# Kernel optimization log

Measured on AMD Instinct MI355X. Metric: run time of the kernel, lower is better.

The kernel has to match this reference:

```python
import jax, jax.numpy as jnp
import numpy as np

INF = 1.0e6  # 'infinity' for squared EDT; max real value is ~3*128^2 ~ 5e4


def edt_1d_sq(f, axis):
    """One pass of Felzenszwalb separable squared EDT along `axis`.
    d[i] = min_j f[j] + (i - j)^2  (brute-force vectorized lower envelope)."""
    f = jnp.moveaxis(f, axis, -1)
    n = f.shape[-1]
    i = jnp.arange(n, dtype=f.dtype)
    sq = (i[:, None] - i[None, :]) ** 2  # (n, n)
    d = jnp.min(f[..., None, :] + sq, axis=-1)  # (..., n)
    return jnp.moveaxis(d, -1, axis)


def compute_fg_dtm(mask):
    """Euclidean distance transform of foreground (distance to nearest background),
    matching scipy.ndimage.distance_transform_edt applied per batch element on the
    (C, X, Y, Z) mask (C==1 so the channel axis pass is the identity).
    mask: bool (B, 1, X, Y, Z) -> float32 (B, 1, X, Y, Z)."""
    def per_b(m):
        g = jnp.where(m, jnp.float32(INF), jnp.float32(0.0))
        for ax in range(m.ndim):
            g = edt_1d_sq(g, ax)
        return jnp.sqrt(g)
    return jax.lax.map(per_b, mask)


def setup_inputs() -> dict:
    key = jax.random.key(0)
    k1, k2, k3 = jax.random.split(key, 3)
    B, C, X, Y, Z = 2, 2, 128, 128, 128
    return {
        "outputs": jax.random.normal(k1, (B, C, X, Y, Z), dtype=jnp.float32),
        "outputs_dist": jax.random.normal(k2, (B, C, X, Y, Z), dtype=jnp.float32) * 10.0,
        "y": jax.random.randint(k3, (B, 1, X, Y, Z), 0, 2),
        "distance_map_weight": 1.0,
    }


def reference(outputs, outputs_dist, y, distance_map_weight):
    n_pred_ch = outputs.shape[1]
    # MONAI one_hot: (B,1,X,Y,Z) int labels -> (B,C,X,Y,Z) float
    y1h = jnp.moveaxis(jax.nn.one_hot(y[:, 0], n_pred_ch, dtype=outputs.dtype), -1, 1)
    x = outputs[:, 1:]            # foreground logits (B, 1, X, Y, Z)
    t = y1h[:, 1:]                # foreground mask
    od = outputs_dist[:, 1:]
    gt_dis = compute_fg_dtm(t > 0.5)
    # BCE with logits (mean reduction), numerically stable
    loss_ce = jnp.mean(jnp.maximum(x, 0.0) - x * t + jnp.log1p(jnp.exp(-jnp.abs(x))))
    # dice loss, flattened per batch element
    N = x.shape[0]
    smooth = jnp.float32(1.0)
    p = jax.nn.sigmoid(x).reshape(N, -1)
    tf = t.reshape(N, -1)
    dice = (2.0 * jnp.sum(p * tf, axis=1) + smooth) / (jnp.sum(p, axis=1) + jnp.sum(tf, axis=1) + smooth)
    loss_dice = 1.0 - jnp.sum(dice) / N
    # weighted L1 on the distance head, masked by the foreground mask
    msum = jnp.sum(t)
    loss_dist = jnp.where(
        msum == 0,
        jnp.float32(0.0),
        jnp.sum(jnp.abs(od - gt_dis) * t) / jnp.maximum(msum, jnp.float32(1e-12)),
    )
    return loss_ce + loss_dice + distance_map_weight * loss_dist
```

## Files before the change

### kernel.cpp

```cpp
#include <hip/hip_runtime.h>
#include <math.h>

#define M_SPATIAL 2097152
#define MV4 (M_SPATIAL / 4)

__device__ __forceinline__ float wave_redf(float v) {
#pragma unroll
  for (int o = 32; o > 0; o >>= 1) v += __shfl_down(v, o, 64);
  return v;
}
__device__ __forceinline__ double wave_redd(double v) {
#pragma unroll
  for (int o = 32; o > 0; o >>= 1) v += __shfl_down(v, o, 64);
  return v;
}


__global__ __launch_bounds__(256) void kA_ce(const float4* __restrict__ outputs4,
                                             const int4* __restrict__ y4,
                                             double* __restrict__ part) {
  int blk = blockIdx.x;
  int base = blk * 1024;
  int b = (blk >= 512) ? 1 : 0;
  const float4* xc = outputs4 + (size_t)(b * 2 + 1) * MV4;
  float ce = 0.f, ps = 0.f, pts = 0.f, tsum = 0.f;
#pragma unroll
  for (int k = 0; k < 4; ++k) {
    int v4 = base + (int)threadIdx.x + k * 256;
    int s4 = v4 & (MV4 - 1);
    int4 yv = y4[v4];
    float4 x = xc[s4];
#define ELEM(c, yc)                                                         \
    {                                                                       \
      float t = (yc == 1) ? 1.0f : 0.0f;                                    \
      float xx = x.c;                                                       \
      ce += fmaxf(xx, 0.0f) - xx * t + log1pf(expf(-fabsf(xx)));            \
      float p = 1.0f / (1.0f + expf(-xx));                                  \
      ps += p; pts += p * t; tsum += t;                                     \
    }
    ELEM(x, yv.x) ELEM(y, yv.y) ELEM(z, yv.z) ELEM(w, yv.w)
#undef ELEM
  }
  float r0 = wave_redf(ce), r1 = wave_redf(ps), r2 = wave_redf(pts), r3 = wave_redf(tsum);
  __shared__ float sm[4][4];
  int lane = threadIdx.x & 63, w = threadIdx.x >> 6;
  if (lane == 0) { sm[w][0] = r0; sm[w][1] = r1; sm[w][2] = r2; sm[w][3] = r3; }
  __syncthreads();
  if (threadIdx.x == 0) {
    part[blk]        = (double)(sm[0][0] + sm[1][0] + sm[2][0] + sm[3][0]);
    part[1024 + blk] = (double)(sm[0][1] + sm[1][1] + sm[2][1] + sm[3][1]);
    part[2048 + blk] = (double)(sm[0][2] + sm[1][2] + sm[2][2] + sm[3][2]);
    part[3072 + blk] = (double)(sm[0][3] + sm[1][3] + sm[2][3] + sm[3][3]);
  }
}

__global__ __launch_bounds__(64) void kB_edtx(const int* __restrict__ y,
                                              float* __restrict__ g) {
  __shared__ int df[128 * 64];
  int blk = blockIdx.x;
  int b  = blk >> 8;
  int yy = (blk >> 1) & 127;
  int zc = blk & 1;
  int l  = threadIdx.x;
  size_t base = (size_t)b * M_SPATIAL + (size_t)yy * 128 + (size_t)zc * 64 + l;

  int d = 200;
  for (int u0 = 0; u0 < 128; u0 += 16) {
    int yb[16];
#pragma unroll
    for (int k = 0; k < 16; ++k) yb[k] = y[base + (size_t)(u0 + k) * 16384];
#pragma unroll
    for (int k = 0; k < 16; ++k) {
      int fg = (yb[k] == 1);
      d = fg ? ((d < 200) ? d + 1 : 200) : 0;
      df[(u0 + k) * 64 + l] = d;
    }
  }
  float hinf = 1000000.f + (float)(yy * yy);
  float yy2f = (float)(yy * yy);
  int db = 200;
  for (int u0 = 127; u0 >= 0; u0 -= 16) {
    int fv[16];
#pragma unroll
    for (int k = 0; k < 16; ++k) fv[k] = df[(u0 - k) * 64 + l];
    float ov[16];
#pragma unroll
    for (int k = 0; k < 16; ++k) {
      db = (fv[k] > 0) ? ((db < 200) ? db + 1 : 200) : 0;
      int m = min(fv[k], db);
      ov[k] = (m >= 128) ? hinf : ((float)(m * m) + yy2f);
    }
#pragma unroll
    for (int k = 0; k < 16; ++k) g[base + (size_t)(u0 - k) * 16384] = ov[k];
  }
}

__global__ __launch_bounds__(256) void kC_edty(float* __restrict__ g) {
  __shared__ float hl[128 * 33];
  int blk = blockIdx.x;
  int b = blk >> 9, xx = (blk >> 2) & 127, zc = blk & 3;
  int t = threadIdx.x;
  size_t rb = (size_t)b * M_SPATIAL + (size_t)xx * 16384 + (size_t)zc * 32;

#pragma unroll
  for (int r = 0; r < 4; ++r) {
    int i4 = t + r * 256;
    int j = i4 >> 3, w = i4 & 7;
    float4 v = *(const float4*)(g + rb + (size_t)j * 128 + 4 * w);
    hl[j * 33 + 4 * w + 0] = v.x;
    hl[j * 33 + 4 * w + 1] = v.y;
    hl[j * 33 + 4 * w + 2] = v.z;
    hl[j * 33 + 4 * w + 3] = v.w;
  }
  __syncthreads();

  int zl = t & 31, ig = t >> 5;
  float best[16], mc[16];
#pragma unroll
  for (int k = 0; k < 16; ++k) {
    best[k] = 3.0e38f;
    mc[k] = -2.0f * (float)(ig * 16 + k);
  }
#pragma unroll 4
  for (int j = 0; j < 128; ++j) {
    float hj = hl[j * 33 + zl];
    float jf = (float)j;
#pragma unroll
    for (int k = 0; k < 16; ++k) best[k] = fminf(best[k], fmaf(mc[k], jf, hj));
  }
  int gz = zc * 32 + zl;
  float zq = (float)(gz * gz);
  size_t ob = rb + zl;
#pragma unroll
  for (int k = 0; k < 16; ++k) {
    int i = ig * 16 + k;
    float dY = (float)(i * i) + best[k];
    g[ob + (size_t)i * 128] = dY + zq;
  }
}

__global__ __launch_bounds__(256) void kD_edtz_dist(const float* __restrict__ g,
                                                    const float* __restrict__ od,
                                                    double* __restrict__ part) {
  __shared__ float hl[128 * 33];
  __shared__ float sred[4];
  int blk = blockIdx.x;
  int b = blk >> 9, xx = (blk >> 2) & 127, yc = blk & 3;
  int t = threadIdx.x;
  size_t rb = (size_t)b * M_SPATIAL + (size_t)xx * 16384 + (size_t)yc * 4096;
  int yl = t & 31, ig = t >> 5;

  size_t odb = (size_t)(2 * b + 1) * M_SPATIAL + (size_t)xx * 16384 +
               (size_t)yc * 4096 + (size_t)yl * 128 + (size_t)ig * 16;
  const float4* o4 = (const float4*)(od + odb);
  float4 ov[4];
#pragma unroll
  for (int r = 0; r < 4; ++r) ov[r] = o4[r];

  const float4* h4 = (const float4*)(g + rb);
#pragma unroll
  for (int r = 0; r < 4; ++r) {
    int i4 = t + r * 256;
    float4 v = h4[i4];
    int flat = i4 * 4;
    int z = flat & 127, yw = flat >> 7;
    hl[(z + 0) * 33 + yw] = v.x;
    hl[(z + 1) * 33 + yw] = v.y;
    hl[(z + 2) * 33 + yw] = v.z;
    hl[(z + 3) * 33 + yw] = v.w;
  }
  __syncthreads();

  float best[16], mc[16];
#pragma unroll
  for (int k = 0; k < 16; ++k) {
    best[k] = 3.0e38f;
    mc[k] = -2.0f * (float)(ig * 16 + k);
  }
#pragma unroll 4
  for (int j = 0; j < 128; ++j) {
    float hj = hl[j * 33 + yl];
    float jf = (float)j;
#pragma unroll
    for (int k = 0; k < 16; ++k) best[k] = fminf(best[k], fmaf(mc[k], jf, hj));
  }
  const float* of = (const float*)ov;
  float dist = 0.f;
#pragma unroll
  for (int k = 0; k < 16; ++k) {
    int i = ig * 16 + k;
    float dv = (float)(i * i) + best[k];
    if (dv > 0.f) dist += fabsf(of[k] - sqrtf(dv));
  }
  float r = wave_redf(dist);
  int lane = t & 63, w = t >> 6;
  if (lane == 0) sred[w] = r;
  __syncthreads();
  if (t == 0) part[4096 + blk] = (double)(sred[0] + sred[1] + sred[2] + sred[3]);
}

__global__ __launch_bounds__(256) void k_final(const double* __restrict__ part,
                                               const float* __restrict__ wptr,
                                               float* __restrict__ out) {
  int i = threadIdx.x;
  double ce  = part[i] + part[i + 256] + part[i + 512] + part[i + 768];
  double p0  = part[1024 + i] + part[1024 + i + 256];
  double p1  = part[1536 + i] + part[1536 + i + 256];
  double pt0 = part[2048 + i] + part[2048 + i + 256];
  double pt1 = part[2560 + i] + part[2560 + i + 256];
  double t0  = part[3072 + i] + part[3072 + i + 256];
  double t1  = part[3584 + i] + part[3584 + i + 256];
  double ds  = part[4096 + i] + part[4096 + i + 256] + part[4096 + i + 512] + part[4096 + i + 768];

  ce = wave_redd(ce); p0 = wave_redd(p0); p1 = wave_redd(p1);
  pt0 = wave_redd(pt0); pt1 = wave_redd(pt1);
  t0 = wave_redd(t0); t1 = wave_redd(t1); ds = wave_redd(ds);

  __shared__ double sm[4][8];
  int lane = threadIdx.x & 63, w = threadIdx.x >> 6;
  if (lane == 0) {
    sm[w][0] = ce; sm[w][1] = p0; sm[w][2] = p1; sm[w][3] = pt0;
    sm[w][4] = pt1; sm[w][5] = t0; sm[w][6] = t1; sm[w][7] = ds;
  }
  __syncthreads();
  if (threadIdx.x == 0) {
    double a[8];
    for (int q = 0; q < 8; ++q) a[q] = sm[0][q] + sm[1][q] + sm[2][q] + sm[3][q];
    double cem = a[0] / 4194304.0;
    double dice0 = (2.0 * a[3] + 1.0) / (a[1] + a[5] + 1.0);
    double dice1 = (2.0 * a[4] + 1.0) / (a[2] + a[6] + 1.0);
    double ldice = 1.0 - 0.5 * (dice0 + dice1);
    double msum = a[5] + a[6];
    double ldist = (msum == 0.0) ? 0.0 : a[7] / fmax(msum, 1e-12);
    out[0] = (float)(cem + ldice + (double)wptr[0] * ldist);
  }
}

extern "C" void kernel_launch(void* const* d_in, const int* in_sizes, int n_in,
                              void* d_out, int out_size, void* d_ws, size_t ws_size,
                              hipStream_t stream) {
  const float* outputs      = (const float*)d_in[0];
  const float* outputs_dist = (const float*)d_in[1];
  const int*   y            = (const int*)d_in[2];
  const float* wptr         = (const float*)d_in[3];
  float* out = (float*)d_out;

  double* part = (double*)d_ws;
  float* g = (float*)((char*)d_ws + 65536);

  kA_ce<<<1024, 256, 0, stream>>>((const float4*)outputs, (const int4*)y, part);
  kB_edtx<<<512, 64, 0, stream>>>(y, g);
  kC_edty<<<1024, 256, 0, stream>>>(g);
  kD_edtz_dist<<<1024, 256, 0, stream>>>(g, outputs_dist, part);
  k_final<<<1, 256, 0, stream>>>(part, wptr, out);
}
```

Baseline: 171.8 us.

## Fuse EDT passes: brute-force X pass from labels, then fused Y+Z pass per slice

Replaces the two-scan X pass with a brute-force lower-envelope pass that reads the labels directly. The Y and Z passes are merged into one kernel that loads a whole 128x128 slice into LDS, does Y, transposes in shared memory, then does Z and the L1 sum. This removes one full global round trip of the intermediate volume and one launch. The cost is more ALU work in the X pass and only 256 blocks of 1024 threads using 64KB of LDS each, which limits occupancy.

```diff
diff --git a/kernel.cpp b/kernel.cpp
--- a/kernel.cpp
+++ b/kernel.cpp
@@ -54,63 +54,24 @@
   }
 }
 
-__global__ __launch_bounds__(64) void kB_edtx(const int* __restrict__ y,
-                                              float* __restrict__ g) {
-  __shared__ int df[128 * 64];
+__global__ __launch_bounds__(256) void kBX_edtx(const int* __restrict__ y,
+                                                float* __restrict__ g) {
+  __shared__ float S[128 * 32];
   int blk = blockIdx.x;
-  int b  = blk >> 8;
-  int yy = (blk >> 1) & 127;
-  int zc = blk & 1;
-  int l  = threadIdx.x;
-  size_t base = (size_t)b * M_SPATIAL + (size_t)yy * 128 + (size_t)zc * 64 + l;
-
-  int d = 200;
-  for (int u0 = 0; u0 < 128; u0 += 16) {
-    int yb[16];
-#pragma unroll
-    for (int k = 0; k < 16; ++k) yb[k] = y[base + (size_t)(u0 + k) * 16384];
-#pragma unroll
-    for (int k = 0; k < 16; ++k) {
-      int fg = (yb[k] == 1);
-      d = fg ? ((d < 200) ? d + 1 : 200) : 0;
-      df[(u0 + k) * 64 + l] = d;
-    }
-  }
-  float hinf = 1000000.f + (float)(yy * yy);
-  float yy2f = (float)(yy * yy);
-  int db = 200;
-  for (int u0 = 127; u0 >= 0; u0 -= 16) {
-    int fv[16];
-#pragma unroll
-    for (int k = 0; k < 16; ++k) fv[k] = df[(u0 - k) * 64 + l];
-    float ov[16];
-#pragma unroll
-    for (int k = 0; k < 16; ++k) {
-      db = (fv[k] > 0) ? ((db < 200) ? db + 1 : 200) : 0;
-      int m = min(fv[k], db);
-      ov[k] = (m >= 128) ? hinf : ((float)(m * m) + yy2f);
-    }
-#pragma unroll
-    for (int k = 0; k < 16; ++k) g[base + (size_t)(u0 - k) * 16384] = ov[k];
-  }
-}
-
-__global__ __launch_bounds__(256) void kC_edty(float* __restrict__ g) {
-  __shared__ float hl[128 * 33];
-  int blk = blockIdx.x;
-  int b = blk >> 9, xx = (blk >> 2) & 127, zc = blk & 3;
+  int b = blk >> 9, yy = (blk >> 2) & 127, zc = blk & 3;
   int t = threadIdx.x;
-  size_t rb = (size_t)b * M_SPATIAL + (size_t)xx * 16384 + (size_t)zc * 32;
+  size_t tb = (size_t)b * M_SPATIAL + (size_t)yy * 128 + (size_t)zc * 32;
 
 #pragma unroll
   for (int r = 0; r < 4; ++r) {
     int i4 = t + r * 256;
-    int j = i4 >> 3, w = i4 & 7;
-    float4 v = *(const float4*)(g + rb + (size_t)j * 128 + 4 * w);
-    hl[j * 33 + 4 * w + 0] = v.x;
-    hl[j * 33 + 4 * w + 1] = v.y;
-    hl[j * 33 + 4 * w + 2] = v.z;
-    hl[j * 33 + 4 * w + 3] = v.w;
+    int j = i4 >> 3, c = (i4 & 7) * 4;
+    const int4 vv = *(const int4*)(y + tb + (size_t)j * 16384 + c);
+    float j2 = (float)(j * j);
+    S[j * 32 + c + 0] = ((vv.x == 1) ? 1000000.f : 0.f) + j2;
+    S[j * 32 + c + 1] = ((vv.y == 1) ? 1000000.f : 0.f) + j2;
+    S[j * 32 + c + 2] = ((vv.z == 1) ? 1000000.f : 0.f) + j2;
+    S[j * 32 + c + 3] = ((vv.w == 1) ? 1000000.f : 0.f) + j2;
   }
   __syncthreads();
 
@@ -123,63 +84,76 @@
   }
 #pragma unroll 4
   for (int j = 0; j < 128; ++j) {
-    float hj = hl[j * 33 + zl];
+    float hj = S[j * 32 + zl];
     float jf = (float)j;
 #pragma unroll
     for (int k = 0; k < 16; ++k) best[k] = fminf(best[k], fmaf(mc[k], jf, hj));
   }
-  int gz = zc * 32 + zl;
-  float zq = (float)(gz * gz);
-  size_t ob = rb + zl;
+  float yq = (float)(yy * yy);
+  size_t ob = tb + zl;
 #pragma unroll
   for (int k = 0; k < 16; ++k) {
     int i = ig * 16 + k;
-    float dY = (float)(i * i) + best[k];
-    g[ob + (size_t)i * 128] = dY + zq;
-  }
-}
-
-__global__ __launch_bounds__(256) void kD_edtz_dist(const float* __restrict__ g,
-                                                    const float* __restrict__ od,
-                                                    double* __restrict__ part) {
-  __shared__ float hl[128 * 33];
-  __shared__ float sred[4];
+    g[ob + (size_t)i * 16384] = (float)(i * i) + best[k] + yq;
+  }
+}
+
+__global__ __launch_bounds__(1024) void kYZ_dist(const float* __restrict__ g,
+                                                 const float* __restrict__ od,
+                                                 double* __restrict__ part) {
+  __shared__ float S[128 * 128];
+  __shared__ float sred[16];
   int blk = blockIdx.x;
-  int b = blk >> 9, xx = (blk >> 2) & 127, yc = blk & 3;
+  int b = blk >> 7, xx = blk & 127;
   int t = threadIdx.x;
-  size_t rb = (size_t)b * M_SPATIAL + (size_t)xx * 16384 + (size_t)yc * 4096;
-  int yl = t & 31, ig = t >> 5;
+  size_t rb = (size_t)b * M_SPATIAL + (size_t)xx * 16384;
+
+  const float4* g4 = (const float4*)(g + rb);
+#pragma unroll
+  for (int r = 0; r < 4; ++r) {
+    int i4 = t + r * 1024;
+    *(float4*)(S + i4 * 4) = g4[i4];
+  }
+  __syncthreads();
+
+  int zl = t & 127, ig = t >> 7;
+  float best[16], mc[16];
+#pragma unroll
+  for (int k = 0; k < 16; ++k) {
+    best[k] = 3.0e38f;
+    mc[k] = -2.0f * (float)(ig * 16 + k);
+  }
+#pragma unroll 4
+  for (int j = 0; j < 128; ++j) {
+    float hj = S[j * 128 + zl];
+    float jf = (float)j;
+#pragma unroll
+    for (int k = 0; k < 16; ++k) best[k] = fminf(best[k], fmaf(mc[k], jf, hj));
+  }
+  float zq = (float)(zl * zl);
+  float outv[16];
+#pragma unroll
+  for (int k = 0; k < 16; ++k) {
+    int i = ig * 16 + k;
+    outv[k] = (float)(i * i) + best[k] + zq;
+  }
+  __syncthreads();
+#pragma unroll
+  for (int k = 0; k < 16; ++k) S[zl * 128 + ig * 16 + k] = outv[k];
+  __syncthreads();
 
   size_t odb = (size_t)(2 * b + 1) * M_SPATIAL + (size_t)xx * 16384 +
-               (size_t)yc * 4096 + (size_t)yl * 128 + (size_t)ig * 16;
+               (size_t)zl * 128 + (size_t)ig * 16;
   const float4* o4 = (const float4*)(od + odb);
   float4 ov[4];
 #pragma unroll
   for (int r = 0; r < 4; ++r) ov[r] = o4[r];
 
-  const float4* h4 = (const float4*)(g + rb);
-#pragma unroll
-  for (int r = 0; r < 4; ++r) {
-    int i4 = t + r * 256;
-    float4 v = h4[i4];
-    int flat = i4 * 4;
-    int z = flat & 127, yw = flat >> 7;
-    hl[(z + 0) * 33 + yw] = v.x;
-    hl[(z + 1) * 33 + yw] = v.y;
-    hl[(z + 2) * 33 + yw] = v.z;
-    hl[(z + 3) * 33 + yw] = v.w;
-  }
-  __syncthreads();
-
-  float best[16], mc[16];
-#pragma unroll
-  for (int k = 0; k < 16; ++k) {
-    best[k] = 3.0e38f;
-    mc[k] = -2.0f * (float)(ig * 16 + k);
-  }
+#pragma unroll
+  for (int k = 0; k < 16; ++k) best[k] = 3.0e38f;
 #pragma unroll 4
   for (int j = 0; j < 128; ++j) {
-    float hj = hl[j * 33 + yl];
+    float hj = S[j * 128 + zl];
     float jf = (float)j;
 #pragma unroll
     for (int k = 0; k < 16; ++k) best[k] = fminf(best[k], fmaf(mc[k], jf, hj));
@@ -196,7 +170,12 @@
   int lane = t & 63, w = t >> 6;
   if (lane == 0) sred[w] = r;
   __syncthreads();
-  if (t == 0) part[4096 + blk] = (double)(sred[0] + sred[1] + sred[2] + sred[3]);
+  if (t == 0) {
+    float s = 0.f;
+#pragma unroll
+    for (int w2 = 0; w2 < 16; ++w2) s += sred[w2];
+    part[4096 + blk] = (double)s;
+  }
 }
 
 __global__ __launch_bounds__(256) void k_final(const double* __restrict__ part,
@@ -210,7 +189,7 @@
   double pt1 = part[2560 + i] + part[2560 + i + 256];
   double t0  = part[3072 + i] + part[3072 + i + 256];
   double t1  = part[3584 + i] + part[3584 + i + 256];
-  double ds  = part[4096 + i] + part[4096 + i + 256] + part[4096 + i + 512] + part[4096 + i + 768];
+  double ds  = part[4096 + i];
 
   ce = wave_redd(ce); p0 = wave_redd(p0); p1 = wave_redd(p1);
   pt0 = wave_redd(pt0); pt1 = wave_redd(pt1);
@@ -249,8 +228,7 @@
   float* g = (float*)((char*)d_ws + 65536);
 
   kA_ce<<<1024, 256, 0, stream>>>((const float4*)outputs, (const int4*)y, part);
-  kB_edtx<<<512, 64, 0, stream>>>(y, g);
-  kC_edty<<<1024, 256, 0, stream>>>(g);
-  kD_edtz_dist<<<1024, 256, 0, stream>>>(g, outputs_dist, part);
+  kBX_edtx<<<1024, 256, 0, stream>>>(y, g);
+  kYZ_dist<<<256, 1024, 0, stream>>>(g, outputs_dist, part);
   k_final<<<1, 256, 0, stream>>>(part, wptr, out);
 }
```

New measurement: 182.1 us. 6.0% more time.
